# Optimization experiments

Hardware: AMD Instinct MI355X
Metric: run time of the kernel (lower is better)

## Reference

```python
import jax, jax.numpy as jnp
import numpy as np

B, T, F = 64, 1000, 512
H, KD = 8, 32
EPS = 1e-6


def setup_inputs() -> dict:
    key = jax.random.key(0)
    ks = jax.random.split(key, 12)
    s_in = 1.0 / np.sqrt(F)
    s_out = 1.0 / np.sqrt(H * KD)
    return {
        "x": jax.random.normal(ks[0], (B, T, F), jnp.float32),
        "q": jax.random.normal(ks[1], (F,), jnp.float32) * s_in,      # global_query (1,1,F) squeezed
        "Wq": jax.random.normal(ks[2], (F, H, KD), jnp.float32) * s_in,
        "bq": jnp.zeros((H, KD), jnp.float32),
        "Wk": jax.random.normal(ks[3], (F, H, KD), jnp.float32) * s_in,
        "bk": jnp.zeros((H, KD), jnp.float32),
        "Wv": jax.random.normal(ks[4], (F, H, KD), jnp.float32) * s_in,
        "bv": jnp.zeros((H, KD), jnp.float32),
        "Wo": jax.random.normal(ks[5], (H, KD, F), jnp.float32) * s_out,
        "bo": jnp.zeros((F,), jnp.float32),
        "Wd": jax.random.normal(ks[6], (F, F), jnp.float32) * s_in,    # Dense, use_bias=False
        "gamma": jnp.ones((F,), jnp.float32),
        "beta": jnp.zeros((F,), jnp.float32),
    }


def reference(x, q, Wq, bq, Wk, bk, Wv, bv, Wo, bo, Wd, gamma, beta):
    # Single learned query attends over full sequence (keras MultiHeadAttention semantics).
    qh = jnp.einsum('f,fhk->hk', q, Wq) + bq                   # (H, KD), shared across batch
    kh = jnp.einsum('btf,fhk->bthk', x, Wk) + bk               # (B, T, H, KD)
    vh = jnp.einsum('btf,fhk->bthk', x, Wv) + bv               # (B, T, H, KD)
    scale = 1.0 / jnp.sqrt(jnp.asarray(KD, x.dtype))
    scores = jnp.einsum('hk,bthk->bht', qh, kh) * scale        # (B, H, T)
    attn = jax.nn.softmax(scores, axis=-1)
    ctx = jnp.einsum('bht,bthk->bhk', attn, vh)                # (B, H, KD)
    pooled = jnp.einsum('bhk,hkf->bf', ctx, Wo) + bo           # (B, F) attention output proj
    out = pooled @ Wd                                          # Dense, no bias
    mu = jnp.mean(out, axis=-1, keepdims=True)
    var = jnp.mean(jnp.square(out - mu), axis=-1, keepdims=True)
    return (out - mu) * jax.lax.rsqrt(var + EPS) * gamma + beta
```

## Files before the change

kernel.cpp:

```cpp
#include <hip/hip_runtime.h>
#include <cstddef>

#define B_ 64
#define T_ 1000
#define F_ 512
#define H_ 8
#define KD_ 32
#define HK_ 256

__global__ __launch_bounds__(64) void k_qh(const float* __restrict__ q,
                                           const float* __restrict__ Wq,
                                           const float* __restrict__ bq,
                                           float* __restrict__ qh) {
    int hk = blockIdx.x;
    int lane = threadIdx.x;
    float s = 0.f;
    for (int f = lane; f < F_; f += 64) s += q[f] * Wq[(size_t)f * HK_ + hk];
    #pragma unroll
    for (int off = 32; off; off >>= 1) s += __shfl_down(s, off);
    if (lane == 0) qh[hk] = s + bq[hk];
}

__global__ __launch_bounds__(256) void k_wk(const float* __restrict__ qh,
                                            const float* __restrict__ Wk,
                                            const float* __restrict__ bk,
                                            float* __restrict__ wk,
                                            float* __restrict__ ck) {
    int f = blockIdx.x;
    int tid = threadIdx.x;
    __shared__ float red[256];
    red[tid] = qh[tid] * Wk[(size_t)f * HK_ + tid];
    __syncthreads();
    #pragma unroll
    for (int off = 16; off; off >>= 1) {
        if ((tid & 31) < off) red[tid] += red[tid + off];
        __syncthreads();
    }
    if ((tid & 31) == 0) wk[f * H_ + (tid >> 5)] = red[tid];
    if (f == 0 && tid < H_) {
        float c = 0.f;
        for (int k = 0; k < KD_; k++) c += qh[tid * KD_ + k] * bk[tid * KD_ + k];
        ck[tid] = c;
    }
}

__global__ __launch_bounds__(256) void k_scores(const float* __restrict__ x,
                                                const float* __restrict__ wk,
                                                const float* __restrict__ ck,
                                                float* __restrict__ scores) {
    int gtid = blockIdx.x * blockDim.x + threadIdx.x;
    int wid = gtid >> 6;
    int lane = threadIdx.x & 63;
    int nw = (gridDim.x * blockDim.x) >> 6;
    int f0 = lane * 8;
    float wreg[8][8];
    #pragma unroll
    for (int i = 0; i < 8; i++)
        #pragma unroll
        for (int h = 0; h < H_; h++) wreg[i][h] = wk[(f0 + i) * H_ + h];
    float ckr[8];
    #pragma unroll
    for (int h = 0; h < H_; h++) ckr[h] = ck[h];
    const float scale = 0.17677669529663687f;

    for (int row = wid; row < B_ * T_; row += nw) {
        const float4* xr = (const float4*)(x + (size_t)row * F_ + f0);
        float4 a = xr[0], bb = xr[1];
        float xv[8] = {a.x, a.y, a.z, a.w, bb.x, bb.y, bb.z, bb.w};
        float acc[8];
        #pragma unroll
        for (int h = 0; h < H_; h++) acc[h] = 0.f;
        #pragma unroll
        for (int i = 0; i < 8; i++)
            #pragma unroll
            for (int h = 0; h < H_; h++) acc[h] += xv[i] * wreg[i][h];
        #pragma unroll
        for (int h = 0; h < H_; h++)
            #pragma unroll
            for (int off = 32; off; off >>= 1) acc[h] += __shfl_xor(acc[h], off);
        if (lane < H_) {
            float v = acc[0];
            #pragma unroll
            for (int h = 1; h < H_; h++) v = (lane == h) ? acc[h] : v;
            int b = row / T_, t = row - b * T_;
            scores[((size_t)b * H_ + lane) * T_ + t] = (v + ckr[lane]) * scale;
        }
    }
}

__global__ __launch_bounds__(256) void k_softmax(float* __restrict__ scores) {
    int row = blockIdx.x;
    int tid = threadIdx.x;
    float* s = scores + (size_t)row * T_;
    __shared__ float red[256];
    float m = -1e30f;
    for (int t = tid; t < T_; t += 256) m = fmaxf(m, s[t]);
    red[tid] = m; __syncthreads();
    #pragma unroll
    for (int off = 128; off; off >>= 1) {
        if (tid < off) red[tid] = fmaxf(red[tid], red[tid + off]);
        __syncthreads();
    }
    m = red[0]; __syncthreads();
    float sum = 0.f;
    for (int t = tid; t < T_; t += 256) { float e = __expf(s[t] - m); s[t] = e; sum += e; }
    red[tid] = sum; __syncthreads();
    #pragma unroll
    for (int off = 128; off; off >>= 1) {
        if (tid < off) red[tid] += red[tid + off];
        __syncthreads();
    }
    float inv = 1.0f / red[0];
    for (int t = tid; t < T_; t += 256) s[t] *= inv;
}

__global__ __launch_bounds__(256) void k_xp(const float* __restrict__ x,
                                            const float* __restrict__ attn,
                                            float* __restrict__ xp_part) {
    int bid = blockIdx.x;
    int tc = bid & 7;
    int b  = bid >> 3;
    int tid = threadIdx.x;
    int t0 = tc * 125;
    __shared__ float at[H_][128];
    for (int i = tid; i < H_ * 128; i += 256) {
        int h = i >> 7, t = i & 127;
        at[h][t] = (t < 125) ? attn[((size_t)b * H_ + h) * T_ + t0 + t] : 0.f;
    }
    __syncthreads();
    float acc[H_][2];
    #pragma unroll
    for (int h = 0; h < H_; h++) { acc[h][0] = 0.f; acc[h][1] = 0.f; }
    const float2* xb = (const float2*)(x + ((size_t)b * T_ + t0) * F_) + tid;
    for (int t = 0; t < 125; t++) {
        float2 xv = xb[(size_t)t * 256];
        #pragma unroll
        for (int h = 0; h < H_; h++) {
            float a = at[h][t];
            acc[h][0] += a * xv.x;
            acc[h][1] += a * xv.y;
        }
    }
    float2* dst = (float2*)(xp_part + ((size_t)(tc * B_ + b) * H_) * F_);
    #pragma unroll
    for (int h = 0; h < H_; h++)
        dst[h * (F_ / 2) + tid] = make_float2(acc[h][0], acc[h][1]);
}

__global__ __launch_bounds__(512) void k_tail(const float* __restrict__ xp_part,
                                              const float* __restrict__ Wv,
                                              const float* __restrict__ bv,
                                              const float* __restrict__ Wo,
                                              const float* __restrict__ bo,
                                              const float* __restrict__ Wd,
                                              const float* __restrict__ gamma,
                                              const float* __restrict__ beta,
                                              float* __restrict__ out) {
    int b = blockIdx.x;
    int tid = threadIdx.x;
    __shared__ float xs[H_ * F_];
    __shared__ float ctx_s[HK_];
    __shared__ float pooled_s[F_];
    __shared__ float red[512];
    __shared__ float stat[2];

    for (int i = tid; i < H_ * F_; i += 512) {
        float s = 0.f;
        #pragma unroll
        for (int p = 0; p < 8; p++)
            s += xp_part[(size_t)(p * B_ + b) * (H_ * F_) + i];
        xs[i] = s;
    }
    __syncthreads();

    {
        int hk = tid & 255;
        int half = tid >> 8;
        int h = hk >> 5;
        float s = 0.f;
        int fb = half * 256;
        for (int j = 0; j < 256; j++) {
            int f = fb + j;
            s += xs[h * F_ + f] * Wv[(size_t)f * HK_ + hk];
        }
        red[tid] = s;
        __syncthreads();
        if (tid < 256) ctx_s[tid] = red[tid] + red[tid + 256] + bv[tid];
    }
    __syncthreads();

    {
        float s = 0.f;
        for (int hk = 0; hk < HK_; hk++) s += ctx_s[hk] * Wo[(size_t)hk * F_ + tid];
        pooled_s[tid] = s + bo[tid];
    }
    __syncthreads();

    float o = 0.f;
    for (int g = 0; g < F_; g++) o += pooled_s[g] * Wd[(size_t)g * F_ + tid];

    {
        float v1 = o, v2 = o * o;
        #pragma unroll
        for (int off = 32; off; off >>= 1) {
            v1 += __shfl_down(v1, off);
            v2 += __shfl_down(v2, off);
        }
        int lane = tid & 63, wid = tid >> 6;
        if (lane == 0) { red[wid] = v1; red[8 + wid] = v2; }
        __syncthreads();
        if (tid == 0) {
            float s1 = 0.f, s2 = 0.f;
            #pragma unroll
            for (int w = 0; w < 8; w++) { s1 += red[w]; s2 += red[8 + w]; }
            float mu = s1 * (1.0f / F_);
            float var = s2 * (1.0f / F_) - mu * mu;
            stat[0] = mu;
            stat[1] = rsqrtf(var + 1e-6f);
        }
        __syncthreads();
    }
    float mu = stat[0], rstd = stat[1];
    out[(size_t)b * F_ + tid] = (o - mu) * rstd * gamma[tid] + beta[tid];
}

extern "C" void kernel_launch(void* const* d_in, const int* in_sizes, int n_in,
                              void* d_out, int out_size, void* d_ws, size_t ws_size,
                              hipStream_t stream) {
    const float* x     = (const float*)d_in[0];
    const float* q     = (const float*)d_in[1];
    const float* Wq    = (const float*)d_in[2];
    const float* bq    = (const float*)d_in[3];
    const float* Wk    = (const float*)d_in[4];
    const float* bk    = (const float*)d_in[5];
    const float* Wv    = (const float*)d_in[6];
    const float* bv    = (const float*)d_in[7];
    const float* Wo    = (const float*)d_in[8];
    const float* bo    = (const float*)d_in[9];
    const float* Wd    = (const float*)d_in[10];
    const float* gamma = (const float*)d_in[11];
    const float* beta  = (const float*)d_in[12];
    float* out = (float*)d_out;

    char* ws = (char*)d_ws;
    float* qh      = (float*)(ws + 0);
    float* wk      = (float*)(ws + 4096);
    float* ck      = (float*)(ws + 20480);
    float* scores  = (float*)(ws + 24576);
    float* xp_part = (float*)(ws + 2097152);

    k_qh<<<HK_, 64, 0, stream>>>(q, Wq, bq, qh);
    k_wk<<<F_, 256, 0, stream>>>(qh, Wk, bk, wk, ck);
    k_scores<<<1024, 256, 0, stream>>>(x, wk, ck, scores);
    k_softmax<<<B_ * H_, 256, 0, stream>>>(scores);
    k_xp<<<B_ * 8, 256, 0, stream>>>(x, scores, xp_part);
    k_tail<<<B_, 512, 0, stream>>>(xp_part, Wv, bv, Wo, bo, Wd, gamma, beta, out);
}
```

Baseline: 301.6 us.

## Fuse scores, softmax and attention-weighted pooling into one split-T kernel

Replaces the separate scores, softmax and x-pooling kernels with one kernel per (batch, T-chunk). Each block computes its chunk's scores and local max and sum, then pools x using unnormalised exponentials while the chunk is still hot in cache. The tail kernel merges the partial results with a log-sum-exp rescale. This removes the scores round trip through global memory and two launches, and x is re-read straight away rather than in a separate pass. In exchange the tail does more reduction work over 16 partial results, and the early phase of each block uses only part of its warps.

```diff
diff --git a/kernel.cpp b/kernel.cpp
--- a/kernel.cpp
+++ b/kernel.cpp
@@ -7,6 +7,7 @@
 #define H_ 8
 #define KD_ 32
 #define HK_ 256
+#define NC_ 16
 
 __global__ __launch_bounds__(64) void k_qh(const float* __restrict__ q,
                                            const float* __restrict__ Wq,
@@ -44,110 +45,104 @@
     }
 }
 
-__global__ __launch_bounds__(256) void k_scores(const float* __restrict__ x,
-                                                const float* __restrict__ wk,
-                                                const float* __restrict__ ck,
-                                                float* __restrict__ scores) {
-    int gtid = blockIdx.x * blockDim.x + threadIdx.x;
-    int wid = gtid >> 6;
-    int lane = threadIdx.x & 63;
-    int nw = (gridDim.x * blockDim.x) >> 6;
-    int f0 = lane * 8;
-    float wreg[8][8];
-    #pragma unroll
-    for (int i = 0; i < 8; i++)
-        #pragma unroll
-        for (int h = 0; h < H_; h++) wreg[i][h] = wk[(f0 + i) * H_ + h];
-    float ckr[8];
-    #pragma unroll
-    for (int h = 0; h < H_; h++) ckr[h] = ck[h];
-    const float scale = 0.17677669529663687f;
-
-    for (int row = wid; row < B_ * T_; row += nw) {
-        const float4* xr = (const float4*)(x + (size_t)row * F_ + f0);
-        float4 a = xr[0], bb = xr[1];
-        float xv[8] = {a.x, a.y, a.z, a.w, bb.x, bb.y, bb.z, bb.w};
-        float acc[8];
-        #pragma unroll
-        for (int h = 0; h < H_; h++) acc[h] = 0.f;
+__global__ __launch_bounds__(256) void k_fused(const float* __restrict__ x,
+                                               const float* __restrict__ wk,
+                                               const float* __restrict__ ck,
+                                               float* __restrict__ part,
+                                               float* __restrict__ ml) {
+    int c = blockIdx.x & (NC_ - 1);
+    int b = blockIdx.x >> 4;
+    int nt = (c < 8) ? 63 : 62;
+    int t0 = (c < 8) ? c * 63 : 504 + (c - 8) * 62;
+    int tid = threadIdx.x;
+    int lane = tid & 63, w = tid >> 6;
+
+    __shared__ float sp[H_][65];
+
+    {
+        int f0 = lane * 8;
+        float wreg[8][8];
         #pragma unroll
         for (int i = 0; i < 8; i++)
             #pragma unroll
-            for (int h = 0; h < H_; h++) acc[h] += xv[i] * wreg[i][h];
+            for (int h = 0; h < H_; h++) wreg[i][h] = wk[(f0 + i) * H_ + h];
+        float ckv = ck[lane >> 3];
+        const float scale = 0.17677669529663687f;
+
+        for (int tl = w; tl < nt; tl += 4) {
+            const float4* xr = (const float4*)(x + ((size_t)(b * T_ + t0 + tl)) * F_ + f0);
+            float4 a = xr[0], bb = xr[1];
+            float xv[8] = {a.x, a.y, a.z, a.w, bb.x, bb.y, bb.z, bb.w};
+            float acc[8];
+            #pragma unroll
+            for (int h = 0; h < H_; h++) acc[h] = 0.f;
+            #pragma unroll
+            for (int i = 0; i < 8; i++)
+                #pragma unroll
+                for (int h = 0; h < H_; h++) acc[h] += xv[i] * wreg[i][h];
+            #pragma unroll
+            for (int h = 0; h < H_; h++) {
+                acc[h] += __shfl_xor(acc[h], 8);
+                acc[h] += __shfl_xor(acc[h], 16);
+                acc[h] += __shfl_xor(acc[h], 32);
+            }
+            float v = acc[0];
+            #pragma unroll
+            for (int h = 1; h < H_; h++) v = ((lane >> 3) == h) ? acc[h] : v;
+            v += __shfl_xor(v, 1);
+            v += __shfl_xor(v, 2);
+            v += __shfl_xor(v, 4);
+            if ((lane & 7) == 0) sp[lane >> 3][tl] = (v + ckv) * scale;
+        }
+    }
+    __syncthreads();
+
+    {
+        int g = tid >> 5, j = tid & 31;
+        float m = -1e30f;
+        #pragma unroll
+        for (int i = 0; i < 2; i++) { int t = j + 32 * i; if (t < nt) m = fmaxf(m, sp[g][t]); }
+        #pragma unroll
+        for (int off = 16; off; off >>= 1) m = fmaxf(m, __shfl_xor(m, off));
+        float l = 0.f;
+        float e0 = 0.f, e1 = 0.f;
+        { int t = j;      if (t < nt) { e0 = __expf(sp[g][t] - m); l += e0; } }
+        { int t = j + 32; if (t < nt) { e1 = __expf(sp[g][t] - m); l += e1; } }
+        __syncthreads();
+        { int t = j;      if (t < nt) sp[g][t] = e0; }
+        { int t = j + 32; if (t < nt) sp[g][t] = e1; }
+        #pragma unroll
+        for (int off = 16; off; off >>= 1) l += __shfl_xor(l, off);
+        if (j == 0) {
+            float* d = ml + ((size_t)(c * B_ + b) * H_ + g) * 2;
+            d[0] = m; d[1] = l;
+        }
+    }
+    __syncthreads();
+
+    {
+        float acc[H_][2];
+        #pragma unroll
+        for (int h = 0; h < H_; h++) { acc[h][0] = 0.f; acc[h][1] = 0.f; }
+        const float2* xb = (const float2*)(x + ((size_t)(b * T_ + t0)) * F_) + tid;
+        for (int tt = 0; tt < nt; tt++) {
+            float2 xv = xb[(size_t)tt * 256];
+            #pragma unroll
+            for (int h = 0; h < H_; h++) {
+                float a = sp[h][tt];
+                acc[h][0] += a * xv.x;
+                acc[h][1] += a * xv.y;
+            }
+        }
+        float2* dst = (float2*)(part + (size_t)(c * B_ + b) * (H_ * F_));
         #pragma unroll
         for (int h = 0; h < H_; h++)
-            #pragma unroll
-            for (int off = 32; off; off >>= 1) acc[h] += __shfl_xor(acc[h], off);
-        if (lane < H_) {
-            float v = acc[0];
-            #pragma unroll
-            for (int h = 1; h < H_; h++) v = (lane == h) ? acc[h] : v;
-            int b = row / T_, t = row - b * T_;
-            scores[((size_t)b * H_ + lane) * T_ + t] = (v + ckr[lane]) * scale;
-        }
-    }
-}
-
-__global__ __launch_bounds__(256) void k_softmax(float* __restrict__ scores) {
-    int row = blockIdx.x;
-    int tid = threadIdx.x;
-    float* s = scores + (size_t)row * T_;
-    __shared__ float red[256];
-    float m = -1e30f;
-    for (int t = tid; t < T_; t += 256) m = fmaxf(m, s[t]);
-    red[tid] = m; __syncthreads();
-    #pragma unroll
-    for (int off = 128; off; off >>= 1) {
-        if (tid < off) red[tid] = fmaxf(red[tid], red[tid + off]);
-        __syncthreads();
-    }
-    m = red[0]; __syncthreads();
-    float sum = 0.f;
-    for (int t = tid; t < T_; t += 256) { float e = __expf(s[t] - m); s[t] = e; sum += e; }
-    red[tid] = sum; __syncthreads();
-    #pragma unroll
-    for (int off = 128; off; off >>= 1) {
-        if (tid < off) red[tid] += red[tid + off];
-        __syncthreads();
-    }
-    float inv = 1.0f / red[0];
-    for (int t = tid; t < T_; t += 256) s[t] *= inv;
-}
-
-__global__ __launch_bounds__(256) void k_xp(const float* __restrict__ x,
-                                            const float* __restrict__ attn,
-                                            float* __restrict__ xp_part) {
-    int bid = blockIdx.x;
-    int tc = bid & 7;
-    int b  = bid >> 3;
-    int tid = threadIdx.x;
-    int t0 = tc * 125;
-    __shared__ float at[H_][128];
-    for (int i = tid; i < H_ * 128; i += 256) {
-        int h = i >> 7, t = i & 127;
-        at[h][t] = (t < 125) ? attn[((size_t)b * H_ + h) * T_ + t0 + t] : 0.f;
-    }
-    __syncthreads();
-    float acc[H_][2];
-    #pragma unroll
-    for (int h = 0; h < H_; h++) { acc[h][0] = 0.f; acc[h][1] = 0.f; }
-    const float2* xb = (const float2*)(x + ((size_t)b * T_ + t0) * F_) + tid;
-    for (int t = 0; t < 125; t++) {
-        float2 xv = xb[(size_t)t * 256];
-        #pragma unroll
-        for (int h = 0; h < H_; h++) {
-            float a = at[h][t];
-            acc[h][0] += a * xv.x;
-            acc[h][1] += a * xv.y;
-        }
-    }
-    float2* dst = (float2*)(xp_part + ((size_t)(tc * B_ + b) * H_) * F_);
-    #pragma unroll
-    for (int h = 0; h < H_; h++)
-        dst[h * (F_ / 2) + tid] = make_float2(acc[h][0], acc[h][1]);
-}
-
-__global__ __launch_bounds__(512) void k_tail(const float* __restrict__ xp_part,
+            dst[h * (F_ / 2) + tid] = make_float2(acc[h][0], acc[h][1]);
+    }
+}
+
+__global__ __launch_bounds__(512) void k_tail(const float* __restrict__ part,
+                                              const float* __restrict__ ml,
                                               const float* __restrict__ Wv,
                                               const float* __restrict__ bv,
                                               const float* __restrict__ Wo,
@@ -158,17 +153,40 @@
                                               float* __restrict__ out) {
     int b = blockIdx.x;
     int tid = threadIdx.x;
+    __shared__ float coefs[NC_][H_];
     __shared__ float xs[H_ * F_];
     __shared__ float ctx_s[HK_];
     __shared__ float pooled_s[F_];
     __shared__ float red[512];
     __shared__ float stat[2];
 
+    if (tid < H_) {
+        int h = tid;
+        float M = -1e30f;
+        #pragma unroll
+        for (int c = 0; c < NC_; c++)
+            M = fmaxf(M, ml[((size_t)(c * B_ + b) * H_ + h) * 2]);
+        float L = 0.f;
+        #pragma unroll
+        for (int c = 0; c < NC_; c++) {
+            const float* d = ml + ((size_t)(c * B_ + b) * H_ + h) * 2;
+            L += __expf(d[0] - M) * d[1];
+        }
+        float invL = 1.0f / L;
+        #pragma unroll
+        for (int c = 0; c < NC_; c++) {
+            const float* d = ml + ((size_t)(c * B_ + b) * H_ + h) * 2;
+            coefs[c][h] = __expf(d[0] - M) * invL;
+        }
+    }
+    __syncthreads();
+
     for (int i = tid; i < H_ * F_; i += 512) {
+        int h = i >> 9;
         float s = 0.f;
         #pragma unroll
-        for (int p = 0; p < 8; p++)
-            s += xp_part[(size_t)(p * B_ + b) * (H_ * F_) + i];
+        for (int c = 0; c < NC_; c++)
+            s += coefs[c][h] * part[(size_t)(c * B_ + b) * (H_ * F_) + i];
         xs[i] = s;
     }
     __syncthreads();
@@ -243,16 +261,14 @@
     float* out = (float*)d_out;
 
     char* ws = (char*)d_ws;
-    float* qh      = (float*)(ws + 0);
-    float* wk      = (float*)(ws + 4096);
-    float* ck      = (float*)(ws + 20480);
-    float* scores  = (float*)(ws + 24576);
-    float* xp_part = (float*)(ws + 2097152);
+    float* qh   = (float*)(ws + 0);
+    float* wk   = (float*)(ws + 4096);
+    float* ck   = (float*)(ws + 20480);
+    float* ml   = (float*)(ws + 24576);
+    float* part = (float*)(ws + 1048576);
 
     k_qh<<<HK_, 64, 0, stream>>>(q, Wq, bq, qh);
     k_wk<<<F_, 256, 0, stream>>>(qh, Wk, bk, wk, ck);
-    k_scores<<<1024, 256, 0, stream>>>(x, wk, ck, scores);
-    k_softmax<<<B_ * H_, 256, 0, stream>>>(scores);
-    k_xp<<<B_ * 8, 256, 0, stream>>>(x, scores, xp_part);
-    k_tail<<<B_, 512, 0, stream>>>(xp_part, Wv, bv, Wo, bo, Wd, gamma, beta, out);
-}
+    k_fused<<<B_ * NC_, 256, 0, stream>>>(x, wk, ck, part, ml);
+    k_tail<<<B_, 512, 0, stream>>>(part, ml, Wv, bv, Wo, bo, Wd, gamma, beta, out);
+}
```

Result: faster. 291.3 us (-3.4%).
